# Performance work log

Hardware: AMD Instinct MI355X
Metric: run time of the kernel (lower is better)

The kernel has to match this reference:

```python
import jax, jax.numpy as jnp
import numpy as np

N = 20000      # nodes
E = 320000     # edges (avg degree 16)
F_IN = 768
DIMS = [(768, 1536), (1536, 768), (768, 384), (384, 256), (256, 5)]


def setup_inputs() -> dict:
    key = jax.random.key(0)
    ks = jax.random.split(key, 2 + 3 * len(DIMS))
    inp = {
        'x': jax.random.normal(ks[0], (N, F_IN), dtype=jnp.float32),
        'edge_index': jax.random.randint(ks[1], (2, E), 0, N, dtype=jnp.int64),
    }
    for li, (fi, fo) in enumerate(DIMS):
        s = 1.0 / np.sqrt(fi)
        inp[f'Wl{li+1}'] = jax.random.uniform(ks[2 + 3 * li], (fi, fo), jnp.float32, -s, s)
        inp[f'Wr{li+1}'] = jax.random.uniform(ks[3 + 3 * li], (fi, fo), jnp.float32, -s, s)
        inp[f'b{li+1}'] = jax.random.uniform(ks[4 + 3 * li], (fo,), jnp.float32, -s, s)
    return inp


def _sage_conv(x, src, dst, deg_inv, Wl, Wr, b):
    # mean aggregate neighbor features, then linear (mean commutes with linear,
    # matching PyG SAGEConv which aggregates x_j then applies lin_l)
    agg = jax.ops.segment_sum(x[src], dst, num_segments=N) * deg_inv  # [N, F_in]
    return agg @ Wl + x @ Wr + b


def reference(x, edge_index,
              Wl1, Wr1, b1, Wl2, Wr2, b2, Wl3, Wr3, b3,
              Wl4, Wr4, b4, Wl5, Wr5, b5):
    src, dst = edge_index[0], edge_index[1]
    deg = jax.ops.segment_sum(jnp.ones((E,), jnp.float32), dst, num_segments=N)
    deg_inv = (1.0 / jnp.maximum(deg, 1.0))[:, None]  # clamp like PyG mean aggr

    h = jax.nn.relu(_sage_conv(x, src, dst, deg_inv, Wl1, Wr1, b1))
    h = jax.nn.relu(_sage_conv(h, src, dst, deg_inv, Wl2, Wr2, b2))
    h = jax.nn.relu(_sage_conv(h, src, dst, deg_inv, Wl3, Wr3, b3))
    h = jax.nn.relu(_sage_conv(h, src, dst, deg_inv, Wl4, Wr4, b4))  # [N, 256]
    out = _sage_conv(h, src, dst, deg_inv, Wl5, Wr5, b5)             # [N, 5]
    return (h, out)
```

## Files before the change

kernel.cpp:

```cpp
#include <hip/hip_runtime.h>
#include <stdint.h>

typedef __attribute__((ext_vector_type(8))) short short8;
typedef __attribute__((ext_vector_type(4))) float f32x4;

__device__ __forceinline__ float bf2f(unsigned short s) {
  return __uint_as_float(((unsigned)s) << 16);
}
__device__ __forceinline__ unsigned short f2bf(float f) {
  unsigned u = __float_as_uint(f);
  u += 0x7fffu + ((u >> 16) & 1u);
  return (unsigned short)(u >> 16);
}

__global__ void gs_zero_i32(int* p, int n) {
  int i = blockIdx.x * 256 + threadIdx.x;
  if (i < n) p[i] = 0;
}

__global__ void gs_count_deg(const int* __restrict__ dst, int* __restrict__ cnt, int E) {
  int e = blockIdx.x * 256 + threadIdx.x;
  if (e < E) atomicAdd(&cnt[dst[e]], 1);
}

__global__ void gs_scanA(const int* __restrict__ cnt, int* __restrict__ rp,
                         int* __restrict__ bsum, int n) {
  __shared__ int sm[256];
  const int b = blockIdx.x, t = threadIdx.x;
  const int base = b * 1024 + t * 4;
  int v[4]; int s = 0;
#pragma unroll
  for (int i = 0; i < 4; ++i) { v[i] = (base + i < n) ? cnt[base + i] : 0; s += v[i]; }
  sm[t] = s;
  __syncthreads();
  for (int off = 1; off < 256; off <<= 1) {
    int x = (t >= off) ? sm[t - off] : 0;
    __syncthreads();
    sm[t] += x;
    __syncthreads();
  }
  int run = sm[t] - s;
#pragma unroll
  for (int i = 0; i < 4; ++i) { if (base + i < n) rp[base + i] = run; run += v[i]; }
  if (t == 255) bsum[b] = sm[255];
}

__global__ void gs_scanB(int* bsum, int nb) {
  if (threadIdx.x == 0 && blockIdx.x == 0) {
    int run = 0;
    for (int i = 0; i < nb; ++i) { int v = bsum[i]; bsum[i] = run; run += v; }
    bsum[nb] = run;
  }
}

__global__ void gs_scanC(int* __restrict__ rp, int* __restrict__ cur,
                         const int* __restrict__ bsum, int n, int nb) {
  int i = blockIdx.x * 256 + threadIdx.x;
  if (i < n) {
    int v = rp[i] + bsum[i >> 10];
    rp[i] = v;
    cur[i] = v;
  }
  if (i == n) rp[n] = bsum[nb];
}

__global__ void gs_fill_csr(const int* __restrict__ src, const int* __restrict__ dst,
                            int* __restrict__ cur, int* __restrict__ col, int E) {
  int e = blockIdx.x * 256 + threadIdx.x;
  if (e < E) {
    int pos = atomicAdd(&cur[dst[e]], 1);
    col[pos] = src[e];
  }
}

__global__ void gs_f32_to_bf16(const float* __restrict__ in, unsigned short* __restrict__ out, int n4) {
  int i = blockIdx.x * 256 + threadIdx.x;
  if (i < n4) {
    float4 f = ((const float4*)in)[i];
    ushort4 o;
    o.x = f2bf(f.x); o.y = f2bf(f.y); o.z = f2bf(f.z); o.w = f2bf(f.w);
    ((ushort4*)out)[i] = o;
  }
}

__global__ void gs_tpack(const float* __restrict__ W, unsigned short* __restrict__ WT,
                         int K, int F) {
  __shared__ float t[32][33];
  const int k0 = blockIdx.x * 32, f0 = blockIdx.y * 32;
  const int tx = threadIdx.x, ty = threadIdx.y;
#pragma unroll
  for (int r = ty; r < 32; r += 8) {
    int k = k0 + r, f = f0 + tx;
    t[r][tx] = (k < K && f < F) ? W[(size_t)k * F + f] : 0.f;
  }
  __syncthreads();
#pragma unroll
  for (int r = ty; r < 32; r += 8) {
    int f = f0 + r, k = k0 + tx;
    if (f < F && k < K) WT[(size_t)f * K + k] = f2bf(t[tx][r]);
  }
}

template <int F, int TPB, int W>
__global__ __launch_bounds__(TPB)
void gs_agg_post(const unsigned short* __restrict__ C, int ldc, int zoff,
                 const int* __restrict__ rp, const int* __restrict__ col,
                 const float* __restrict__ bias,
                 unsigned short* __restrict__ hout, float* __restrict__ fout, int relu) {
  static_assert(TPB * W == F, "layout");
  const int v = blockIdx.x;
  const int tid = threadIdx.x;
  const int s0 = rp[v], s1 = rp[v + 1];
  const float inv = 1.0f / (float)max(s1 - s0, 1);
  float acc[W];
#pragma unroll
  for (int w = 0; w < W; ++w) acc[w] = 0.f;

  __shared__ int nb[TPB];
  for (int base = s0; base < s1; base += TPB) {
    int m = min(s1 - base, TPB);
    __syncthreads();
    if (tid < m) nb[tid] = col[base + tid];
    __syncthreads();
    int j = 0;
    for (; j + 4 <= m; j += 4) {
      const unsigned short* x0 = C + (size_t)nb[j + 0] * ldc + tid * W;
      const unsigned short* x1 = C + (size_t)nb[j + 1] * ldc + tid * W;
      const unsigned short* x2 = C + (size_t)nb[j + 2] * ldc + tid * W;
      const unsigned short* x3 = C + (size_t)nb[j + 3] * ldc + tid * W;
      if constexpr (W == 4) {
        ushort4 u0 = *(const ushort4*)x0;
        ushort4 u1 = *(const ushort4*)x1;
        ushort4 u2 = *(const ushort4*)x2;
        ushort4 u3 = *(const ushort4*)x3;
        acc[0] += bf2f(u0.x) + bf2f(u1.x) + bf2f(u2.x) + bf2f(u3.x);
        acc[1] += bf2f(u0.y) + bf2f(u1.y) + bf2f(u2.y) + bf2f(u3.y);
        acc[2] += bf2f(u0.z) + bf2f(u1.z) + bf2f(u2.z) + bf2f(u3.z);
        acc[3] += bf2f(u0.w) + bf2f(u1.w) + bf2f(u2.w) + bf2f(u3.w);
      } else {
        ushort2 u0 = *(const ushort2*)x0;
        ushort2 u1 = *(const ushort2*)x1;
        ushort2 u2 = *(const ushort2*)x2;
        ushort2 u3 = *(const ushort2*)x3;
        acc[0] += bf2f(u0.x) + bf2f(u1.x) + bf2f(u2.x) + bf2f(u3.x);
        acc[1] += bf2f(u0.y) + bf2f(u1.y) + bf2f(u2.y) + bf2f(u3.y);
      }
    }
    for (; j < m; ++j) {
      const unsigned short* xr = C + (size_t)nb[j] * ldc + tid * W;
      if constexpr (W == 4) {
        ushort4 u = *(const ushort4*)xr;
        acc[0] += bf2f(u.x); acc[1] += bf2f(u.y); acc[2] += bf2f(u.z); acc[3] += bf2f(u.w);
      } else {
        ushort2 u = *(const ushort2*)xr;
        acc[0] += bf2f(u.x); acc[1] += bf2f(u.y);
      }
    }
  }

  float o[W];
#pragma unroll
  for (int w = 0; w < W; ++w) o[w] = acc[w] * inv;
  if (zoff >= 0) {
    const unsigned short* zr = C + (size_t)v * ldc + zoff + tid * W;
    if constexpr (W == 4) {
      ushort4 u = *(const ushort4*)zr;
      o[0] += bf2f(u.x); o[1] += bf2f(u.y); o[2] += bf2f(u.z); o[3] += bf2f(u.w);
    } else {
      ushort2 u = *(const ushort2*)zr;
      o[0] += bf2f(u.x); o[1] += bf2f(u.y);
    }
  }
  if (bias) {
#pragma unroll
    for (int w = 0; w < W; ++w) o[w] += bias[tid * W + w];
  }
  if (relu) {
#pragma unroll
    for (int w = 0; w < W; ++w) o[w] = fmaxf(o[w], 0.f);
  }
  if (hout) {
    if constexpr (W == 4) {
      ushort4 u; u.x = f2bf(o[0]); u.y = f2bf(o[1]); u.z = f2bf(o[2]); u.w = f2bf(o[3]);
      *(ushort4*)(hout + (size_t)v * F + tid * W) = u;
    } else {
      ushort2 u; u.x = f2bf(o[0]); u.y = f2bf(o[1]);
      *(ushort2*)(hout + (size_t)v * F + tid * W) = u;
    }
  }
  if (fout) {
    if constexpr (W == 4) {
      *(float4*)(fout + (size_t)v * F + tid * W) = make_float4(o[0], o[1], o[2], o[3]);
    } else {
      *(float2*)(fout + (size_t)v * F + tid * W) = make_float2(o[0], o[1]);
    }
  }
}

__global__ __launch_bounds__(256)
void gs_gemm(const unsigned short* __restrict__ A1, const unsigned short* __restrict__ A2,
             const unsigned short* __restrict__ B1, const unsigned short* __restrict__ B2,
             const float* __restrict__ bias, unsigned short* __restrict__ Hout,
             int M, int Nn, int K, int doRelu, int Mt, int Nt) {
  __shared__ unsigned short lA[128 * 64];
  __shared__ unsigned short lB[128 * 64];
  const int tid = threadIdx.x;
  const int wid = tid >> 6;
  const int lane = tid & 63;

  const int MG = 8;
  const int per = MG * Nt;
  const int g = blockIdx.x / per;
  const int rem = blockIdx.x - g * per;
  const int gsz = min(MG, Mt - g * MG);
  const int nIdx = rem / gsz;
  const int mIdx = g * MG + (rem - nIdx * gsz);
  const int bM = mIdx * 128;
  const int bN = nIdx * 128;
  const int wM = (wid >> 1) * 64;
  const int wN = (wid & 1) * 64;

  f32x4 acc[4][4];
#pragma unroll
  for (int i = 0; i < 4; ++i)
#pragma unroll
    for (int j = 0; j < 4; ++j) acc[i][j] = (f32x4){0.f, 0.f, 0.f, 0.f};

  const int mrow = wM + (lane & 15);
  const int nrow = wN + (lane & 15);
  const int q = lane >> 4;
  const int swz = lane & 7;
  const int srow = wid * 8 + (lane >> 3);
  const int sc = (lane & 7) ^ (lane >> 3);
  const int npass = A2 ? 2 : 1;

  for (int pass = 0; pass < npass; ++pass) {
    const unsigned short* Ap = pass ? A2 : A1;
    const unsigned short* Bp = pass ? B2 : B1;
    for (int k0 = 0; k0 < K; k0 += 64) {
#pragma unroll
      for (int r = 0; r < 4; ++r) {
        int row = r * 32 + srow;
        int ga = bM + row;
        if (ga >= M) ga = M - 1;
        const unsigned short* gpA = Ap + (size_t)ga * K + k0 + sc * 8;
        const unsigned short* gpB = Bp + (size_t)(bN + row) * K + k0 + sc * 8;
        unsigned lo = (unsigned)(r * 32 + wid * 8) * 128;
        __builtin_amdgcn_global_load_lds(
            (const __attribute__((address_space(1))) unsigned int*)gpA,
            (__attribute__((address_space(3))) unsigned int*)((char*)lA + lo), 16, 0, 0);
        __builtin_amdgcn_global_load_lds(
            (const __attribute__((address_space(1))) unsigned int*)gpB,
            (__attribute__((address_space(3))) unsigned int*)((char*)lB + lo), 16, 0, 0);
      }
      __syncthreads();
#pragma unroll
      for (int s = 0; s < 2; ++s) {
        const int cofs = ((s * 4 + q) ^ swz) * 8;
        short8 aF[4], bF[4];
#pragma unroll
        for (int i = 0; i < 4; ++i) {
          aF[i] = *(const short8*)&lA[(mrow + i * 16) * 64 + cofs];
          bF[i] = *(const short8*)&lB[(nrow + i * 16) * 64 + cofs];
        }
#pragma unroll
        for (int i = 0; i < 4; ++i)
#pragma unroll
          for (int j = 0; j < 4; ++j)
            acc[i][j] = __builtin_amdgcn_mfma_f32_16x16x32_bf16(aF[i], bF[j], acc[i][j], 0, 0, 0);
      }
      __syncthreads();
    }
  }

  const int rbase = bM + wM + (lane >> 4) * 4;
#pragma unroll
  for (int i = 0; i < 4; ++i) {
#pragma unroll
    for (int r = 0; r < 4; ++r) {
      int row = rbase + i * 16 + r;
      if (row >= M) continue;
#pragma unroll
      for (int j = 0; j < 4; ++j) {
        int colN = bN + wN + j * 16 + (lane & 15);
        float v = acc[i][j][r];
        if (bias) v += bias[colN];
        if (doRelu) v = fmaxf(v, 0.f);
        Hout[(size_t)row * Nn + colN] = f2bf(v);
      }
    }
  }
}

__global__ __launch_bounds__(64)
void gs_l5dot(const unsigned short* __restrict__ h4, const float* __restrict__ Wl,
              const float* __restrict__ Wr, float* __restrict__ yz) {
  __shared__ float sW[2560];
  const int v = blockIdx.x;
  const int l = threadIdx.x;
  for (int i = l; i < 2560; i += 64) sW[i] = (i < 1280) ? Wl[i] : Wr[i - 1280];
  __syncthreads();
  ushort4 u = ((const ushort4*)(h4 + (size_t)v * 256))[l];
  float hv[4] = {bf2f(u.x), bf2f(u.y), bf2f(u.z), bf2f(u.w)};
  float acc[10];
#pragma unroll
  for (int n = 0; n < 10; ++n) acc[n] = 0.f;
#pragma unroll
  for (int t = 0; t < 4; ++t) {
    int k = 4 * l + t;
#pragma unroll
    for (int n = 0; n < 5; ++n) {
      acc[n] += hv[t] * sW[k * 5 + n];
      acc[5 + n] += hv[t] * sW[1280 + k * 5 + n];
    }
  }
#pragma unroll
  for (int n = 0; n < 10; ++n)
    for (int off = 32; off > 0; off >>= 1) acc[n] += __shfl_down(acc[n], off, 64);
  if (l == 0) {
#pragma unroll
    for (int n = 0; n < 10; ++n) yz[(size_t)v * 10 + n] = acc[n];
  }
}

__global__ __launch_bounds__(64)
void gs_l5agg(const float* __restrict__ yz, const int* __restrict__ rp,
              const int* __restrict__ col, const float* __restrict__ b,
              float* __restrict__ out) {
  const int v = blockIdx.x;
  const int l = threadIdx.x;
  const int s0 = rp[v], s1 = rp[v + 1];
  const float inv = 1.0f / (float)max(s1 - s0, 1);
  float acc[5] = {0.f, 0.f, 0.f, 0.f, 0.f};
  for (int e = s0 + l; e < s1; e += 64) {
    const float* yr = yz + (size_t)col[e] * 10;
#pragma unroll
    for (int n = 0; n < 5; ++n) acc[n] += yr[n];
  }
#pragma unroll
  for (int n = 0; n < 5; ++n)
    for (int off = 32; off > 0; off >>= 1) acc[n] += __shfl_down(acc[n], off, 64);
  if (l == 0) {
#pragma unroll
    for (int n = 0; n < 5; ++n)
      out[(size_t)v * 5 + n] = acc[n] * inv + yz[(size_t)v * 10 + 5 + n] + b[n];
  }
}

extern "C" void kernel_launch(void* const* d_in, const int* in_sizes, int n_in,
                              void* d_out, int out_size, void* d_ws, size_t ws_size,
                              hipStream_t stream) {
  const float* x = (const float*)d_in[0];
  const int* ei = (const int*)d_in[1];
  const int N = in_sizes[0] / 768;
  const int E = in_sizes[1] / 2;
  const int* src = ei;
  const int* dst = ei + E;

  const float* Wl[5];
  const float* Wr[5];
  const float* bb[5];
  for (int l = 0; l < 5; ++l) {
    Wl[l] = (const float*)d_in[2 + 3 * l];
    Wr[l] = (const float*)d_in[3 + 3 * l];
    bb[l] = (const float*)d_in[4 + 3 * l];
  }

  char* w = (char*)d_ws;
  size_t off = 0;
  auto take = [&](size_t bytes) -> char* {
    char* p = w + off;
    off = (off + bytes + 255) & ~(size_t)255;
    return p;
  };
  unsigned short* ar1 = (unsigned short*)take((size_t)N * 768 * 2);
  unsigned short* ar2 = (unsigned short*)take((size_t)N * 768 * 2);
  unsigned short* ar3 = (unsigned short*)take((size_t)N * 1536 * 2);
  unsigned short* C2  = (unsigned short*)take((size_t)N * 1536 * 2);
  int* cnt  = (int*)take((size_t)N * 4);
  int* rp   = (int*)take((size_t)(N + 1) * 4);
  int* cur  = (int*)take((size_t)N * 4);
  int* col  = (int*)take((size_t)E * 4);
  const int nbChunks = (N + 1023) / 1024;
  int* bsum = (int*)take((size_t)(nbChunks + 1) * 4);
  unsigned short* WT1l = (unsigned short*)take((size_t)1536 * 768 * 2);
  unsigned short* WT1r = (unsigned short*)take((size_t)1536 * 768 * 2);
  unsigned short* WT2  = (unsigned short*)take((size_t)1536 * 1536 * 2);
  unsigned short* WT3  = (unsigned short*)take((size_t)768 * 768 * 2);
  unsigned short* WT4  = (unsigned short*)take((size_t)512 * 384 * 2);

  unsigned short* xb   = ar1;
  unsigned short* C3   = ar1;
  unsigned short* aggb = ar2;
  unsigned short* h2   = ar2;
  unsigned short* h1   = ar3;
  unsigned short* C4   = ar3;
  unsigned short* h3   = ar3 + (size_t)N * 512;
  unsigned short* h4   = ar3 + (size_t)N * (512 + 384);
  float*          yz5  = (float*)(ar3 + (size_t)N * (512 + 384 + 256));

  const int M = N;
  const int Mt = (M + 127) / 128;

  gs_zero_i32<<<(N + 255) / 256, 256, 0, stream>>>(cnt, N);
  gs_count_deg<<<(E + 255) / 256, 256, 0, stream>>>(dst, cnt, E);
  gs_scanA<<<nbChunks, 256, 0, stream>>>(cnt, rp, bsum, N);
  gs_scanB<<<1, 64, 0, stream>>>(bsum, nbChunks);
  gs_scanC<<<(N + 256) / 256, 256, 0, stream>>>(rp, cur, bsum, N, nbChunks);
  gs_fill_csr<<<(E + 255) / 256, 256, 0, stream>>>(src, dst, cur, col, E);

  gs_f32_to_bf16<<<((N * 768 / 4) + 255) / 256, 256, 0, stream>>>(x, xb, N * 768 / 4);
  gs_tpack<<<dim3(24, 48), dim3(32, 8), 0, stream>>>(Wl[0], WT1l, 768, 1536);
  gs_tpack<<<dim3(24, 48), dim3(32, 8), 0, stream>>>(Wr[0], WT1r, 768, 1536);
  gs_tpack<<<dim3(48, 24), dim3(32, 8), 0, stream>>>(Wl[1], WT2, 1536, 768);
  gs_tpack<<<dim3(48, 24), dim3(32, 8), 0, stream>>>(Wr[1], WT2 + (size_t)768 * 1536, 1536, 768);
  gs_tpack<<<dim3(24, 12), dim3(32, 8), 0, stream>>>(Wl[2], WT3, 768, 384);
  gs_tpack<<<dim3(24, 12), dim3(32, 8), 0, stream>>>(Wr[2], WT3 + (size_t)384 * 768, 768, 384);
  gs_tpack<<<dim3(12, 8), dim3(32, 8), 0, stream>>>(Wl[3], WT4, 384, 256);
  gs_tpack<<<dim3(12, 8), dim3(32, 8), 0, stream>>>(Wr[3], WT4 + (size_t)256 * 384, 384, 256);

  float* houtF = (float*)d_out;
  float* out5  = (float*)d_out + (size_t)N * 256;

  gs_agg_post<768, 192, 4><<<N, 192, 0, stream>>>(xb, 768, -1, rp, col, nullptr, aggb, nullptr, 0);
  gs_gemm<<<Mt * 12, 256, 0, stream>>>(aggb, xb, WT1l, WT1r, bb[0], h1, M, 1536, 768, 1, Mt, 12);

  gs_gemm<<<Mt * 12, 256, 0, stream>>>(h1, nullptr, WT2, nullptr, nullptr, C2, M, 1536, 1536, 0, Mt, 12);
  gs_agg_post<768, 192, 4><<<N, 192, 0, stream>>>(C2, 1536, 768, rp, col, bb[1], h2, nullptr, 1);

  gs_gemm<<<Mt * 6, 256, 0, stream>>>(h2, nullptr, WT3, nullptr, nullptr, C3, M, 768, 768, 0, Mt, 6);
  gs_agg_post<384, 192, 2><<<N, 192, 0, stream>>>(C3, 768, 384, rp, col, bb[2], h3, nullptr, 1);

  gs_gemm<<<Mt * 4, 256, 0, stream>>>(h3, nullptr, WT4, nullptr, nullptr, C4, M, 512, 384, 0, Mt, 4);
  gs_agg_post<256, 64, 4><<<N, 64, 0, stream>>>(C4, 512, 256, rp, col, bb[3], h4, houtF, 1);

  gs_l5dot<<<N, 64, 0, stream>>>(h4, Wl[4], Wr[4], yz5);
  gs_l5agg<<<N, 64, 0, stream>>>(yz5, rp, col, bb[4], out5);
}
```

Before: 727.1 us.

## Split aggregation into 128-column wave slices, batch weight packing, memset counts

Replaces the per-node aggregation kernel (one block of 192 or 64 threads per node) with a 64-thread kernel where each wave handles a 128-column slice of one node, using a 2D grid (node, slice). The eight weight-transpose launches are merged into one launch that reads its per-block arguments from a struct, and the zeroing kernel becomes hipMemsetAsync. The aim is more, smaller blocks for better scheduling of the gather-heavy aggregation and fewer launches. In exchange, neighbor indices are loaded once per slice instead of once per node, and each lane loads only 2 bf16 values, which may lower memory efficiency. Many blocks in the merged transpose launch exit early.

```diff
diff --git a/kernel.cpp b/kernel.cpp
--- a/kernel.cpp
+++ b/kernel.cpp
@@ -11,11 +11,6 @@
   unsigned u = __float_as_uint(f);
   u += 0x7fffu + ((u >> 16) & 1u);
   return (unsigned short)(u >> 16);
-}
-
-__global__ void gs_zero_i32(int* p, int n) {
-  int i = blockIdx.x * 256 + threadIdx.x;
-  if (i < n) p[i] = 0;
 }
 
 __global__ void gs_count_deg(const int* __restrict__ dst, int* __restrict__ cnt, int E) {
@@ -83,118 +78,72 @@
   }
 }
 
-__global__ void gs_tpack(const float* __restrict__ W, unsigned short* __restrict__ WT,
-                         int K, int F) {
+struct TP { const float* W; unsigned short* WT; int K, F; };
+struct TP8 { TP t[8]; };
+
+__global__ void gs_tpack8(TP8 args) {
+  const TP a = args.t[blockIdx.z];
+  const int k0 = blockIdx.x * 32, f0 = blockIdx.y * 32;
+  if (k0 >= a.K || f0 >= a.F) return;
   __shared__ float t[32][33];
-  const int k0 = blockIdx.x * 32, f0 = blockIdx.y * 32;
   const int tx = threadIdx.x, ty = threadIdx.y;
 #pragma unroll
   for (int r = ty; r < 32; r += 8) {
     int k = k0 + r, f = f0 + tx;
-    t[r][tx] = (k < K && f < F) ? W[(size_t)k * F + f] : 0.f;
+    t[r][tx] = (k < a.K && f < a.F) ? a.W[(size_t)k * a.F + f] : 0.f;
   }
   __syncthreads();
 #pragma unroll
   for (int r = ty; r < 32; r += 8) {
     int f = f0 + r, k = k0 + tx;
-    if (f < F && k < K) WT[(size_t)f * K + k] = f2bf(t[tx][r]);
-  }
-}
-
-template <int F, int TPB, int W>
-__global__ __launch_bounds__(TPB)
-void gs_agg_post(const unsigned short* __restrict__ C, int ldc, int zoff,
-                 const int* __restrict__ rp, const int* __restrict__ col,
-                 const float* __restrict__ bias,
-                 unsigned short* __restrict__ hout, float* __restrict__ fout, int relu) {
-  static_assert(TPB * W == F, "layout");
+    if (f < a.F && k < a.K) a.WT[(size_t)f * a.K + k] = f2bf(t[tx][r]);
+  }
+}
+
+__global__ __launch_bounds__(64)
+void gs_agg_slice(const unsigned short* __restrict__ C, int ldc, int zoff,
+                  const int* __restrict__ rp, const int* __restrict__ col,
+                  const float* __restrict__ bias,
+                  unsigned short* __restrict__ hout, float* __restrict__ fout,
+                  int F, int relu) {
   const int v = blockIdx.x;
-  const int tid = threadIdx.x;
+  const int cc = blockIdx.y * 128 + 2 * threadIdx.x;
+  const int l = threadIdx.x;
   const int s0 = rp[v], s1 = rp[v + 1];
   const float inv = 1.0f / (float)max(s1 - s0, 1);
-  float acc[W];
-#pragma unroll
-  for (int w = 0; w < W; ++w) acc[w] = 0.f;
-
-  __shared__ int nb[TPB];
-  for (int base = s0; base < s1; base += TPB) {
-    int m = min(s1 - base, TPB);
+  float a0 = 0.f, a1 = 0.f;
+  __shared__ int nb[64];
+  for (int base = s0; base < s1; base += 64) {
+    int m = min(s1 - base, 64);
     __syncthreads();
-    if (tid < m) nb[tid] = col[base + tid];
+    if (l < m) nb[l] = col[base + l];
     __syncthreads();
     int j = 0;
     for (; j + 4 <= m; j += 4) {
-      const unsigned short* x0 = C + (size_t)nb[j + 0] * ldc + tid * W;
-      const unsigned short* x1 = C + (size_t)nb[j + 1] * ldc + tid * W;
-      const unsigned short* x2 = C + (size_t)nb[j + 2] * ldc + tid * W;
-      const unsigned short* x3 = C + (size_t)nb[j + 3] * ldc + tid * W;
-      if constexpr (W == 4) {
-        ushort4 u0 = *(const ushort4*)x0;
-        ushort4 u1 = *(const ushort4*)x1;
-        ushort4 u2 = *(const ushort4*)x2;
-        ushort4 u3 = *(const ushort4*)x3;
-        acc[0] += bf2f(u0.x) + bf2f(u1.x) + bf2f(u2.x) + bf2f(u3.x);
-        acc[1] += bf2f(u0.y) + bf2f(u1.y) + bf2f(u2.y) + bf2f(u3.y);
-        acc[2] += bf2f(u0.z) + bf2f(u1.z) + bf2f(u2.z) + bf2f(u3.z);
-        acc[3] += bf2f(u0.w) + bf2f(u1.w) + bf2f(u2.w) + bf2f(u3.w);
-      } else {
-        ushort2 u0 = *(const ushort2*)x0;
-        ushort2 u1 = *(const ushort2*)x1;
-        ushort2 u2 = *(const ushort2*)x2;
-        ushort2 u3 = *(const ushort2*)x3;
-        acc[0] += bf2f(u0.x) + bf2f(u1.x) + bf2f(u2.x) + bf2f(u3.x);
-        acc[1] += bf2f(u0.y) + bf2f(u1.y) + bf2f(u2.y) + bf2f(u3.y);
-      }
+      ushort2 u0 = *(const ushort2*)(C + (size_t)nb[j + 0] * ldc + cc);
+      ushort2 u1 = *(const ushort2*)(C + (size_t)nb[j + 1] * ldc + cc);
+      ushort2 u2 = *(const ushort2*)(C + (size_t)nb[j + 2] * ldc + cc);
+      ushort2 u3 = *(const ushort2*)(C + (size_t)nb[j + 3] * ldc + cc);
+      a0 += bf2f(u0.x) + bf2f(u1.x) + bf2f(u2.x) + bf2f(u3.x);
+      a1 += bf2f(u0.y) + bf2f(u1.y) + bf2f(u2.y) + bf2f(u3.y);
     }
     for (; j < m; ++j) {
-      const unsigned short* xr = C + (size_t)nb[j] * ldc + tid * W;
-      if constexpr (W == 4) {
-        ushort4 u = *(const ushort4*)xr;
-        acc[0] += bf2f(u.x); acc[1] += bf2f(u.y); acc[2] += bf2f(u.z); acc[3] += bf2f(u.w);
-      } else {
-        ushort2 u = *(const ushort2*)xr;
-        acc[0] += bf2f(u.x); acc[1] += bf2f(u.y);
-      }
-    }
-  }
-
-  float o[W];
-#pragma unroll
-  for (int w = 0; w < W; ++w) o[w] = acc[w] * inv;
+      ushort2 u = *(const ushort2*)(C + (size_t)nb[j] * ldc + cc);
+      a0 += bf2f(u.x); a1 += bf2f(u.y);
+    }
+  }
+  float o0 = a0 * inv, o1 = a1 * inv;
   if (zoff >= 0) {
-    const unsigned short* zr = C + (size_t)v * ldc + zoff + tid * W;
-    if constexpr (W == 4) {
-      ushort4 u = *(const ushort4*)zr;
-      o[0] += bf2f(u.x); o[1] += bf2f(u.y); o[2] += bf2f(u.z); o[3] += bf2f(u.w);
-    } else {
-      ushort2 u = *(const ushort2*)zr;
-      o[0] += bf2f(u.x); o[1] += bf2f(u.y);
-    }
-  }
-  if (bias) {
-#pragma unroll
-    for (int w = 0; w < W; ++w) o[w] += bias[tid * W + w];
-  }
-  if (relu) {
-#pragma unroll
-    for (int w = 0; w < W; ++w) o[w] = fmaxf(o[w], 0.f);
-  }
+    ushort2 u = *(const ushort2*)(C + (size_t)v * ldc + zoff + cc);
+    o0 += bf2f(u.x); o1 += bf2f(u.y);
+  }
+  if (bias) { o0 += bias[cc]; o1 += bias[cc + 1]; }
+  if (relu) { o0 = fmaxf(o0, 0.f); o1 = fmaxf(o1, 0.f); }
   if (hout) {
-    if constexpr (W == 4) {
-      ushort4 u; u.x = f2bf(o[0]); u.y = f2bf(o[1]); u.z = f2bf(o[2]); u.w = f2bf(o[3]);
-      *(ushort4*)(hout + (size_t)v * F + tid * W) = u;
-    } else {
-      ushort2 u; u.x = f2bf(o[0]); u.y = f2bf(o[1]);
-      *(ushort2*)(hout + (size_t)v * F + tid * W) = u;
-    }
-  }
-  if (fout) {
-    if constexpr (W == 4) {
-      *(float4*)(fout + (size_t)v * F + tid * W) = make_float4(o[0], o[1], o[2], o[3]);
-    } else {
-      *(float2*)(fout + (size_t)v * F + tid * W) = make_float2(o[0], o[1]);
-    }
-  }
+    ushort2 u; u.x = f2bf(o0); u.y = f2bf(o1);
+    *(ushort2*)(hout + (size_t)v * F + cc) = u;
+  }
+  if (fout) *(float2*)(fout + (size_t)v * F + cc) = make_float2(o0, o1);
 }
 
 __global__ __launch_bounds__(256)
@@ -402,7 +351,7 @@
   const int M = N;
   const int Mt = (M + 127) / 128;
 
-  gs_zero_i32<<<(N + 255) / 256, 256, 0, stream>>>(cnt, N);
+  hipMemsetAsync(cnt, 0, (size_t)N * 4, stream);
   gs_count_deg<<<(E + 255) / 256, 256, 0, stream>>>(dst, cnt, E);
   gs_scanA<<<nbChunks, 256, 0, stream>>>(cnt, rp, bsum, N);
   gs_scanB<<<1, 64, 0, stream>>>(bsum, nbChunks);
@@ -410,29 +359,31 @@
   gs_fill_csr<<<(E + 255) / 256, 256, 0, stream>>>(src, dst, cur, col, E);
 
   gs_f32_to_bf16<<<((N * 768 / 4) + 255) / 256, 256, 0, stream>>>(x, xb, N * 768 / 4);
-  gs_tpack<<<dim3(24, 48), dim3(32, 8), 0, stream>>>(Wl[0], WT1l, 768, 1536);
-  gs_tpack<<<dim3(24, 48), dim3(32, 8), 0, stream>>>(Wr[0], WT1r, 768, 1536);
-  gs_tpack<<<dim3(48, 24), dim3(32, 8), 0, stream>>>(Wl[1], WT2, 1536, 768);
-  gs_tpack<<<dim3(48, 24), dim3(32, 8), 0, stream>>>(Wr[1], WT2 + (size_t)768 * 1536, 1536, 768);
-  gs_tpack<<<dim3(24, 12), dim3(32, 8), 0, stream>>>(Wl[2], WT3, 768, 384);
-  gs_tpack<<<dim3(24, 12), dim3(32, 8), 0, stream>>>(Wr[2], WT3 + (size_t)384 * 768, 768, 384);
-  gs_tpack<<<dim3(12, 8), dim3(32, 8), 0, stream>>>(Wl[3], WT4, 384, 256);
-  gs_tpack<<<dim3(12, 8), dim3(32, 8), 0, stream>>>(Wr[3], WT4 + (size_t)256 * 384, 384, 256);
+  TP8 tp;
+  tp.t[0] = {Wl[0], WT1l, 768, 1536};
+  tp.t[1] = {Wr[0], WT1r, 768, 1536};
+  tp.t[2] = {Wl[1], WT2, 1536, 768};
+  tp.t[3] = {Wr[1], WT2 + (size_t)768 * 1536, 1536, 768};
+  tp.t[4] = {Wl[2], WT3, 768, 384};
+  tp.t[5] = {Wr[2], WT3 + (size_t)384 * 768, 768, 384};
+  tp.t[6] = {Wl[3], WT4, 384, 256};
+  tp.t[7] = {Wr[3], WT4 + (size_t)256 * 384, 384, 256};
+  gs_tpack8<<<dim3(48, 48, 8), dim3(32, 8), 0, stream>>>(tp);
 
   float* houtF = (float*)d_out;
   float* out5  = (float*)d_out + (size_t)N * 256;
 
-  gs_agg_post<768, 192, 4><<<N, 192, 0, stream>>>(xb, 768, -1, rp, col, nullptr, aggb, nullptr, 0);
+  gs_agg_slice<<<dim3(N, 6), 64, 0, stream>>>(xb, 768, -1, rp, col, nullptr, aggb, nullptr, 768, 0);
   gs_gemm<<<Mt * 12, 256, 0, stream>>>(aggb, xb, WT1l, WT1r, bb[0], h1, M, 1536, 768, 1, Mt, 12);
 
   gs_gemm<<<Mt * 12, 256, 0, stream>>>(h1, nullptr, WT2, nullptr, nullptr, C2, M, 1536, 1536, 0, Mt, 12);
-  gs_agg_post<768, 192, 4><<<N, 192, 0, stream>>>(C2, 1536, 768, rp, col, bb[1], h2, nullptr, 1);
+  gs_agg_slice<<<dim3(N, 6), 64, 0, stream>>>(C2, 1536, 768, rp, col, bb[1], h2, nullptr, 768, 1);
 
   gs_gemm<<<Mt * 6, 256, 0, stream>>>(h2, nullptr, WT3, nullptr, nullptr, C3, M, 768, 768, 0, Mt, 6);
-  gs_agg_post<384, 192, 2><<<N, 192, 0, stream>>>(C3, 768, 384, rp, col, bb[2], h3, nullptr, 1);
+  gs_agg_slice<<<dim3(N, 3), 64, 0, stream>>>(C3, 768, 384, rp, col, bb[2], h3, nullptr, 384, 1);
 
   gs_gemm<<<Mt * 4, 256, 0, stream>>>(h3, nullptr, WT4, nullptr, nullptr, C4, M, 512, 384, 0, Mt, 4);
-  gs_agg_post<256, 64, 4><<<N, 64, 0, stream>>>(C4, 512, 256, rp, col, bb[3], h4, houtF, 1);
+  gs_agg_slice<<<dim3(N, 2), 64, 0, stream>>>(C4, 512, 256, rp, col, bb[3], h4, houtF, 256, 1);
 
   gs_l5dot<<<N, 64, 0, stream>>>(h4, Wl[4], Wr[4], yz5);
   gs_l5agg<<<N, 64, 0, stream>>>(yz5, rp, col, bb[4], out5);
```

Result: faster. 687.1 us (-5.5%).
